# Optimization experiments

Measured on AMD Instinct MI355X. Metric: run time of the kernel, lower is better.

The kernel has to match this reference:

```python
import jax, jax.numpy as jnp
import numpy as np

N, E, SEQ, IN, HID, OUT = 2048, 65536, 5, 32, 64, 16
EPS = 1e-5


def setup_inputs() -> dict:
    ks = jax.random.split(jax.random.key(0), 16)
    def w(k, shape):
        return jax.random.normal(k, shape, jnp.float32) / np.float32(np.sqrt(shape[0]))
    z = lambda n: jnp.zeros((n,), jnp.float32)
    return dict(
        x=jax.random.normal(ks[0], (SEQ, N, IN), jnp.float32),
        edge_weight=jax.random.uniform(ks[1], (E,), jnp.float32),
        Wcz=w(ks[2], (IN, HID)), bcz=z(HID), Wlz=w(ks[3], (2 * HID, HID)), blz=z(HID),
        Wcr=w(ks[4], (IN, HID)), bcr=z(HID), Wlr=w(ks[5], (2 * HID, HID)), blr=z(HID),
        Wch=w(ks[6], (IN, HID)), bch=z(HID), Wlh=w(ks[7], (2 * HID, HID)), blh=z(HID),
        Wred=w(ks[8], (SEQ * HID, HID)), bred=z(HID),
        Wc1=w(ks[9], (HID, HID)), bc1=z(HID), Wc2=w(ks[10], (HID, HID)), bc2=z(HID),
        g1=jnp.ones((HID,), jnp.float32), be1=z(HID),
        g2=jnp.ones((HID,), jnp.float32), be2=z(HID),
        Wout=w(ks[11], (HID, OUT)), bout=z(OUT),
        Wi1=w(ks[12], (2 * HID, HID)), bi1=z(HID),
        Wi2=w(ks[13], (HID, 1)), bi2=z(1),
        edge_index=jax.random.randint(ks[14], (2, E), 0, N),
    )


def _layer_norm(h, g, b):
    mu = jnp.mean(h, -1, keepdims=True)
    var = jnp.mean((h - mu) ** 2, -1, keepdims=True)
    return (h - mu) * jax.lax.rsqrt(var + EPS) * g + b


def _forward(x, edge_weight, Wcz, bcz, Wlz, blz, Wcr, bcr, Wlr, blr,
             Wch, bch, Wlh, blh, Wred, bred, Wc1, bc1, Wc2, bc2,
             g1, be1, g2, be2, Wout, bout, Wi1, bi1, Wi2, bi2, edge_index):
    src, dst = edge_index[0], edge_index[1]
    # GCN symmetric normalization with self-loops (weight 1.0); shared by all convs.
    deg = jax.ops.segment_sum(edge_weight, dst, num_segments=N) + 1.0
    dinv = jax.lax.rsqrt(deg)
    norm = dinv[src] * edge_weight * dinv[dst]  # [E]
    dself = dinv * dinv                          # [N] self-loop coefficient

    def gcn(h, W, b):
        hw = h @ W
        agg = jax.ops.segment_sum(norm[:, None] * hw[src], dst, num_segments=N)
        return agg + dself[:, None] * hw + b

    # TGCN per timestep. The original passes no hidden state, so H resets to 0
    # each call: H_t = (1 - Z) * tanh(candidate); reset gate R is multiplied by
    # H=0 and has no effect (its params get zero gradient, matching torch).
    hs = []
    for t in range(SEQ):  # SEQ=5, fixed small loop
        Zg = jax.nn.sigmoid(gcn(x[t], Wcz, bcz) @ Wlz[:HID] + blz)
        Ht = jnp.tanh(gcn(x[t], Wch, bch) @ Wlh[:HID] + blh)
        hs.append((1.0 - Zg) * Ht)
    h = jnp.stack(hs, axis=1).reshape(N, SEQ * HID)
    h = h @ Wred + bred
    emb = h  # intermediate embeddings for the interaction predictor
    h = gcn(h, Wc1, bc1)
    h = jax.nn.relu(_layer_norm(h, g1, be1))  # dropout = identity in eval
    h = gcn(h, Wc2, bc2)
    h = jax.nn.relu(_layer_norm(h, g2, be2))
    node_pred = h @ Wout + bout
    # InteractionPredictor: cat([e_i, e_j]) @ Wi1 == e_i @ Wi1[:H] + e_j @ Wi1[H:]
    a = emb @ Wi1[:HID]
    bj = emb @ Wi1[HID:]
    hp = jax.nn.relu(a[:, None, :] + bj[None, :, :] + bi1)  # [N, N, HID]
    scores = (hp @ Wi2)[..., 0] + bi2[0]                     # [N, N]
    return node_pred, scores


def reference(x, edge_index, edge_weight, Wcz, bcz, Wlz, blz, Wcr, bcr, Wlr, blr,
              Wch, bch, Wlh, blh, Wred, bred, Wc1, bc1, Wc2, bc2,
              g1, be1, g2, be2, Wout, bout, Wi1, bi1, Wi2, bi2):
    return _forward(x, edge_weight, Wcz, bcz, Wlz, blz, Wcr, bcr, Wlr, blr,
                    Wch, bch, Wlh, blh, Wred, bred, Wc1, bc1, Wc2, bc2,
                    g1, be1, g2, be2, Wout, bout, Wi1, bi1, Wi2, bi2, edge_index)
```

## Files before the change

### kernel.cpp

```cpp
#include <hip/hip_runtime.h>
#include <math.h>

#define N_NODES 2048
#define N_EDGES 65536
#define SEQL 5
#define IN_F 32
#define HID 64
#define OUT_F 16
#define LN_EPS 1e-5f

__global__ void k_deg(const int* __restrict__ ei, const float* __restrict__ ew,
                      float* __restrict__ deg, int* __restrict__ cnt){
    int e = blockIdx.x * 256 + threadIdx.x;
    if (e < N_EDGES){
        int d = ei[N_EDGES + e];
        atomicAdd(&deg[d], ew[e]);
        atomicAdd(&cnt[d], 1);
    }
}

__global__ void k_scan_wcomb(const float* __restrict__ deg, const int* __restrict__ cnt,
                             float* __restrict__ dinv, float* __restrict__ dself, int* __restrict__ rowptr,
                             const float* __restrict__ Wcz, const float* __restrict__ Wlz,
                             const float* __restrict__ bcz, const float* __restrict__ blz,
                             const float* __restrict__ Wch, const float* __restrict__ Wlh,
                             const float* __restrict__ bch, const float* __restrict__ blh,
                             float* __restrict__ Wzp, float* __restrict__ Whp, float* __restrict__ bUV){
    int b = blockIdx.x, t = threadIdx.x;
    if (b == 0){
        __shared__ int s[1024];
        int n0 = 2*t, n1 = 2*t + 1;
        float d0 = deg[n0] + 1.f, d1 = deg[n1] + 1.f;
        float i0 = 1.f / sqrtf(d0), i1 = 1.f / sqrtf(d1);
        dinv[n0] = i0; dinv[n1] = i1;
        dself[n0] = i0*i0; dself[n1] = i1*i1;
        int a0 = cnt[n0], a1 = cnt[n1];
        s[t] = a0 + a1;
        __syncthreads();
        for (int off = 1; off < 1024; off <<= 1){
            int v = (t >= off) ? s[t - off] : 0;
            __syncthreads();
            s[t] += v;
            __syncthreads();
        }
        int pe = (t == 0) ? 0 : s[t-1];
        rowptr[n0] = pe;
        rowptr[n1] = pe + a0;
        if (t == 1023) rowptr[2048] = s[1023];
    } else {
        const float* Wc = (b == 1) ? Wcz : Wch;
        const float* Wl = (b == 1) ? Wlz : Wlh;
        const float* bc = (b == 1) ? bcz : bch;
        const float* bl = (b == 1) ? blz : blh;
        float* Wp = (b == 1) ? Wzp : Whp;
        for (int idx = t; idx < IN_F*HID; idx += 1024){
            int i = idx >> 6, f = idx & 63;
            float s = 0.f;
            for (int k = 0; k < HID; ++k) s += Wc[i*HID+k] * Wl[k*HID+f];
            Wp[idx] = s;
        }
        if (t < HID){
            float s = bl[t];
            for (int k = 0; k < HID; ++k) s += bc[k] * Wl[k*HID+t];
            bUV[(b-1)*HID + t] = s;
        }
    }
}

__global__ void k_csr(const int* __restrict__ ei, const float* __restrict__ ew,
                      const float* __restrict__ dinv, const int* __restrict__ rowptr,
                      int* __restrict__ fill, int* __restrict__ csrc, float* __restrict__ cnrm){
    int e = blockIdx.x * 256 + threadIdx.x;
    if (e < N_EDGES){
        int s = ei[e], d = ei[N_EDGES + e];
        int pos = rowptr[d] + atomicAdd(&fill[d], 1);
        csrc[pos] = s;
        cnrm[pos] = dinv[s] * ew[e] * dinv[d];
    }
}

__global__ void k_uv(const float* __restrict__ x, const float* __restrict__ Wzp,
                     const float* __restrict__ Whp, float* __restrict__ U, float* __restrict__ V){
    int r = blockIdx.x;
    int t = threadIdx.x;
    __shared__ float xs[IN_F];
    if (t < IN_F) xs[t] = x[r*IN_F + t];
    __syncthreads();
    int f = t & 63;
    const float* W = (t < 64) ? Wzp : Whp;
    float* O = (t < 64) ? U : V;
    float s = 0.f;
    #pragma unroll
    for (int i = 0; i < IN_F; ++i) s += xs[i] * W[i*HID + f];
    O[r*HID + f] = s;
}

__global__ __launch_bounds__(320) void k_gate(
                       const float* __restrict__ U, const float* __restrict__ V, const float* __restrict__ bUV,
                       const float* __restrict__ dself, const int* __restrict__ rowptr,
                       const int* __restrict__ csrc, const float* __restrict__ cnrm,
                       const float* __restrict__ Wred, const float* __restrict__ bred,
                       const float* __restrict__ Wi1, const float* __restrict__ bi1, const float* __restrict__ Wc1,
                       float* __restrict__ emb, float* __restrict__ ag, float* __restrict__ bjp,
                       float* __restrict__ hw1){
    int n = blockIdx.x;
    int f = threadIdx.x & 63;
    int t = threadIdx.x >> 6;
    __shared__ float hs[SEQL][HID];
    __shared__ float part[SEQL][HID];
    float ds = dself[n];
    int beg = rowptr[n], end = rowptr[n+1];
    const float* Ut = U + (size_t)t * N_NODES * HID;
    const float* Vt = V + (size_t)t * N_NODES * HID;
    float au = 0.f, av = 0.f;
    int p = beg;
    for (; p + 1 < end; p += 2){
        int   s0 = csrc[p],  s1 = csrc[p+1];
        float n0 = cnrm[p],  n1 = cnrm[p+1];
        float u0 = Ut[s0*HID+f], u1 = Ut[s1*HID+f];
        float v0 = Vt[s0*HID+f], v1 = Vt[s1*HID+f];
        au += n0*u0 + n1*u1;
        av += n0*v0 + n1*v1;
    }
    if (p < end){
        int s0 = csrc[p]; float n0 = cnrm[p];
        au += n0 * Ut[s0*HID+f];
        av += n0 * Vt[s0*HID+f];
    }
    float zz = au + ds * Ut[n*HID+f] + bUV[f];
    float hh = av + ds * Vt[n*HID+f] + bUV[HID+f];
    float z = 1.f / (1.f + expf(-zz));
    hs[t][f] = (1.f - z) * tanhf(hh);
    __syncthreads();
    float pp = 0.f;
    #pragma unroll
    for (int k = 0; k < HID; ++k) pp += hs[t][k] * Wred[(t*HID + k)*HID + f];
    part[t][f] = pp;
    __syncthreads();
    if (t == 0){
        float hred = bred[f] + part[0][f] + part[1][f] + part[2][f] + part[3][f] + part[4][f];
        emb[n*HID + f] = hred;
        hs[0][f] = hred;
    }
    __syncthreads();
    if (t < 3){
        const float* W = (t == 0) ? Wi1 : (t == 1) ? (Wi1 + HID*HID) : Wc1;
        float acc = (t == 1) ? bi1[f] : 0.f;
        #pragma unroll
        for (int k = 0; k < HID; ++k) acc += hs[0][k] * W[k*HID + f];
        float* O = (t == 0) ? ag : (t == 1) ? bjp : hw1;
        O[n*HID + f] = acc;
    }
}

__global__ __launch_bounds__(256) void k_gcn1(
                       const float* __restrict__ hw1, const float* __restrict__ dself,
                       const int* __restrict__ rowptr, const int* __restrict__ csrc, const float* __restrict__ cnrm,
                       const float* __restrict__ bc1, const float* __restrict__ g1, const float* __restrict__ be1,
                       const float* __restrict__ Wc2, float* __restrict__ hw2){
    int n = blockIdx.x;
    int f = threadIdx.x & 63;
    int w = threadIdx.x >> 6;
    int beg = rowptr[n], end = rowptr[n+1];
    __shared__ float red[4][HID];
    __shared__ float hsh[HID];
    float agg = 0.f;
    for (int p = beg + w; p < end; p += 4) agg += cnrm[p] * hw1[csrc[p]*HID + f];
    red[w][f] = agg;
    __syncthreads();
    if (w == 0){
        float g = red[0][f] + red[1][f] + red[2][f] + red[3][f]
                + dself[n] * hw1[n*HID + f] + bc1[f];
        float sum = g;
        for (int o = 32; o > 0; o >>= 1) sum += __shfl_xor(sum, o, 64);
        float mu = sum * (1.f/64.f);
        float d = g - mu;
        float vs = d * d;
        for (int o = 32; o > 0; o >>= 1) vs += __shfl_xor(vs, o, 64);
        float var = vs * (1.f/64.f);
        float h = d * (1.f / sqrtf(var + LN_EPS)) * g1[f] + be1[f];
        hsh[f] = fmaxf(h, 0.f);
    }
    __syncthreads();
    float s = 0.f;
    #pragma unroll
    for (int k = 0; k < 16; ++k) s += hsh[w*16 + k] * Wc2[(w*16 + k)*HID + f];
    red[w][f] = s;
    __syncthreads();
    if (w == 0) hw2[n*HID + f] = red[0][f] + red[1][f] + red[2][f] + red[3][f];
}

__global__ __launch_bounds__(256) void k_gcn2(
                       const float* __restrict__ hw2, const float* __restrict__ dself,
                       const int* __restrict__ rowptr, const int* __restrict__ csrc, const float* __restrict__ cnrm,
                       const float* __restrict__ bc2, const float* __restrict__ g2, const float* __restrict__ be2,
                       const float* __restrict__ Wout, const float* __restrict__ bout, float* __restrict__ outp){
    int n = blockIdx.x;
    int f = threadIdx.x & 63;
    int w = threadIdx.x >> 6;
    int beg = rowptr[n], end = rowptr[n+1];
    __shared__ float red[4][HID];
    __shared__ float hsh[HID];
    float agg = 0.f;
    for (int p = beg + w; p < end; p += 4) agg += cnrm[p] * hw2[csrc[p]*HID + f];
    red[w][f] = agg;
    __syncthreads();
    if (w == 0){
        float g = red[0][f] + red[1][f] + red[2][f] + red[3][f]
                + dself[n] * hw2[n*HID + f] + bc2[f];
        float sum = g;
        for (int o = 32; o > 0; o >>= 1) sum += __shfl_xor(sum, o, 64);
        float mu = sum * (1.f/64.f);
        float d = g - mu;
        float vs = d * d;
        for (int o = 32; o > 0; o >>= 1) vs += __shfl_xor(vs, o, 64);
        float var = vs * (1.f/64.f);
        float h = d * (1.f / sqrtf(var + LN_EPS)) * g2[f] + be2[f];
        hsh[f] = fmaxf(h, 0.f);
    }
    __syncthreads();
    if (w == 0 && f < OUT_F){
        float s = bout[f];
        #pragma unroll
        for (int k = 0; k < HID; ++k) s += hsh[k] * Wout[k*OUT_F + f];
        outp[n*OUT_F + f] = s;
    }
}

__global__ __launch_bounds__(256) void k_scores(const float* __restrict__ ag, const float* __restrict__ bjp,
                         const float* __restrict__ Wi2, const float* __restrict__ bi2,
                         float* __restrict__ outs){
    __shared__ float bs[64*65];
    __shared__ float wv[64];
    int tid = threadIdx.x;
    int j0 = blockIdx.x * 64;
    int i0 = blockIdx.y * 16;
    for (int idx = tid; idx < 4096; idx += 256){
        int jj = idx >> 6, f = idx & 63;
        bs[jj*65 + f] = bjp[(j0 + jj)*HID + f];
    }
    if (tid < 64) wv[tid] = Wi2[tid];
    __syncthreads();
    int tj = tid & 63;
    int w = __builtin_amdgcn_readfirstlane(tid >> 6);
    const float* ar = ag + (i0 + w*4)*HID;
    float bi2v = bi2[0];
    float acc0 = 0.f, acc1 = 0.f, acc2 = 0.f, acc3 = 0.f;
    #pragma unroll
    for (int f = 0; f < 64; ++f){
        float bv = bs[tj*65 + f];
        float wf = wv[f];
        acc0 += fmaxf(ar[       f] + bv, 0.f) * wf;
        acc1 += fmaxf(ar[ 64 +  f] + bv, 0.f) * wf;
        acc2 += fmaxf(ar[128 +  f] + bv, 0.f) * wf;
        acc3 += fmaxf(ar[192 +  f] + bv, 0.f) * wf;
    }
    long ro = (long)(i0 + w*4) * N_NODES + j0 + tj;
    outs[ro                ] = acc0 + bi2v;
    outs[ro +     N_NODES  ] = acc1 + bi2v;
    outs[ro + 2L* N_NODES  ] = acc2 + bi2v;
    outs[ro + 3L* N_NODES  ] = acc3 + bi2v;
}

extern "C" void kernel_launch(void* const* d_in, const int* in_sizes, int n_in,
                              void* d_out, int out_size, void* d_ws, size_t ws_size,
                              hipStream_t stream){
    const float* x   = (const float*)d_in[0];
    const float* ew  = (const float*)d_in[1];
    const float* Wcz = (const float*)d_in[2];  const float* bcz = (const float*)d_in[3];
    const float* Wlz = (const float*)d_in[4];  const float* blz = (const float*)d_in[5];
    const float* Wch = (const float*)d_in[10]; const float* bch = (const float*)d_in[11];
    const float* Wlh = (const float*)d_in[12]; const float* blh = (const float*)d_in[13];
    const float* Wred= (const float*)d_in[14]; const float* bred= (const float*)d_in[15];
    const float* Wc1 = (const float*)d_in[16]; const float* bc1 = (const float*)d_in[17];
    const float* Wc2 = (const float*)d_in[18]; const float* bc2 = (const float*)d_in[19];
    const float* g1  = (const float*)d_in[20]; const float* be1 = (const float*)d_in[21];
    const float* g2  = (const float*)d_in[22]; const float* be2 = (const float*)d_in[23];
    const float* Wout= (const float*)d_in[24]; const float* bout= (const float*)d_in[25];
    const float* Wi1 = (const float*)d_in[26]; const float* bi1 = (const float*)d_in[27];
    const float* Wi2 = (const float*)d_in[28]; const float* bi2 = (const float*)d_in[29];
    const int*  ei  = (const int*)d_in[30];

    char* w = (char*)d_ws;
    float* deg    = (float*)(w + 0);
    int*   cnt    = (int*)  (w + 8192);
    int*   fill   = (int*)  (w + 16384);
    int*   rowptr = (int*)  (w + 24576);
    float* dinv   = (float*)(w + 36864);
    float* dself  = (float*)(w + 45056);
    int*   csrc   = (int*)  (w + 53248);
    float* cnrm   = (float*)(w + 315392);
    float* Wzp    = (float*)(w + 577536);
    float* Whp    = (float*)(w + 585728);
    float* bUV    = (float*)(w + 593920);
    float* U      = (float*)(w + 595968);
    float* V      = (float*)(w + 595968 + 2621440);
    float* emb    = (float*)(w + 595968 + 2*2621440);
    float* ag     = emb + N_NODES*HID;
    float* bjp    = ag  + N_NODES*HID;
    float* hw1    = bjp + N_NODES*HID;
    float* hw2    = hw1 + N_NODES*HID;

    hipMemsetAsync(d_ws, 0, 24576, stream);
    k_deg<<<N_EDGES/256, 256, 0, stream>>>(ei, ew, deg, cnt);
    k_scan_wcomb<<<3, 1024, 0, stream>>>(deg, cnt, dinv, dself, rowptr,
                                         Wcz, Wlz, bcz, blz, Wch, Wlh, bch, blh,
                                         Wzp, Whp, bUV);
    k_csr<<<N_EDGES/256, 256, 0, stream>>>(ei, ew, dinv, rowptr, fill, csrc, cnrm);
    k_uv<<<SEQL*N_NODES, 128, 0, stream>>>(x, Wzp, Whp, U, V);
    k_gate<<<N_NODES, 320, 0, stream>>>(U, V, bUV, dself, rowptr, csrc, cnrm,
                                        Wred, bred, Wi1, bi1, Wc1,
                                        emb, ag, bjp, hw1);
    k_gcn1<<<N_NODES, 256, 0, stream>>>(hw1, dself, rowptr, csrc, cnrm, bc1, g1, be1, Wc2, hw2);
    k_gcn2<<<N_NODES, 256, 0, stream>>>(hw2, dself, rowptr, csrc, cnrm, bc2, g2, be2, Wout, bout,
                                        (float*)d_out);
    dim3 sg(N_NODES/64, N_NODES/16);
    k_scores<<<sg, 256, 0, stream>>>(ag, bjp, Wi2, bi2, (float*)d_out + N_NODES*OUT_F);
}
```

Baseline: 231.7 us.

## Aggregate raw inputs before projection and vectorize scores kernel LDS loads

Uses the linearity of the GCN to aggregate the 32-wide input features over neighbours first (k_aggx), then applies the combined Z/H projections inside the gate kernel. This drops the separate U/V projection kernel and halves the gather width from two 64-wide tensors per timestep to one 32-wide tensor, removing the U/V intermediate buffers. The scores kernel also stages the ag rows in shared memory with float4 loads and reads operands as float4 from padded LDS. The trade-off is extra per-node projection arithmetic in the gate kernel, plus floating-point summation order changing slightly.

```diff
diff --git a/kernel.cpp b/kernel.cpp
--- a/kernel.cpp
+++ b/kernel.cpp
@@ -79,56 +79,54 @@
     }
 }
 
-__global__ void k_uv(const float* __restrict__ x, const float* __restrict__ Wzp,
-                     const float* __restrict__ Whp, float* __restrict__ U, float* __restrict__ V){
-    int r = blockIdx.x;
-    int t = threadIdx.x;
-    __shared__ float xs[IN_F];
-    if (t < IN_F) xs[t] = x[r*IN_F + t];
-    __syncthreads();
-    int f = t & 63;
-    const float* W = (t < 64) ? Wzp : Whp;
-    float* O = (t < 64) ? U : V;
-    float s = 0.f;
-    #pragma unroll
-    for (int i = 0; i < IN_F; ++i) s += xs[i] * W[i*HID + f];
-    O[r*HID + f] = s;
-}
-
-__global__ __launch_bounds__(320) void k_gate(
-                       const float* __restrict__ U, const float* __restrict__ V, const float* __restrict__ bUV,
-                       const float* __restrict__ dself, const int* __restrict__ rowptr,
-                       const int* __restrict__ csrc, const float* __restrict__ cnrm,
-                       const float* __restrict__ Wred, const float* __restrict__ bred,
-                       const float* __restrict__ Wi1, const float* __restrict__ bi1, const float* __restrict__ Wc1,
-                       float* __restrict__ emb, float* __restrict__ ag, float* __restrict__ bjp,
-                       float* __restrict__ hw1){
+__global__ __launch_bounds__(256) void k_aggx(const float* __restrict__ x, const float* __restrict__ dself,
+        const int* __restrict__ rowptr, const int* __restrict__ csrc, const float* __restrict__ cnrm,
+        float* __restrict__ aggX){
+    int n = blockIdx.x;
+    int tid = threadIdx.x;
+    int slot = tid >> 5, f = tid & 31;
+    __shared__ float part[8][SEQL][IN_F];
+    float acc[SEQL] = {0.f, 0.f, 0.f, 0.f, 0.f};
+    int beg = rowptr[n], end = rowptr[n+1];
+    for (int p = beg + slot; p < end; p += 8){
+        int s = csrc[p]; float c = cnrm[p];
+        #pragma unroll
+        for (int t = 0; t < SEQL; ++t)
+            acc[t] += c * x[(t*N_NODES + s)*IN_F + f];
+    }
+    #pragma unroll
+    for (int t = 0; t < SEQL; ++t) part[slot][t][f] = acc[t];
+    __syncthreads();
+    if (tid < SEQL*IN_F){
+        int t = tid >> 5, ff = tid & 31;
+        float s = dself[n] * x[(t*N_NODES + n)*IN_F + ff];
+        #pragma unroll
+        for (int sl = 0; sl < 8; ++sl) s += part[sl][t][ff];
+        aggX[n*(SEQL*IN_F) + tid] = s;
+    }
+}
+
+__global__ __launch_bounds__(320) void k_gate2(const float* __restrict__ aggX, const float* __restrict__ bUV,
+        const float* __restrict__ Wzp, const float* __restrict__ Whp,
+        const float* __restrict__ Wred, const float* __restrict__ bred,
+        const float* __restrict__ Wi1, const float* __restrict__ bi1, const float* __restrict__ Wc1,
+        float* __restrict__ emb, float* __restrict__ ag, float* __restrict__ bjp,
+        float* __restrict__ hw1){
     int n = blockIdx.x;
     int f = threadIdx.x & 63;
     int t = threadIdx.x >> 6;
+    __shared__ float axs[SEQL][IN_F];
     __shared__ float hs[SEQL][HID];
     __shared__ float part[SEQL][HID];
-    float ds = dself[n];
-    int beg = rowptr[n], end = rowptr[n+1];
-    const float* Ut = U + (size_t)t * N_NODES * HID;
-    const float* Vt = V + (size_t)t * N_NODES * HID;
-    float au = 0.f, av = 0.f;
-    int p = beg;
-    for (; p + 1 < end; p += 2){
-        int   s0 = csrc[p],  s1 = csrc[p+1];
-        float n0 = cnrm[p],  n1 = cnrm[p+1];
-        float u0 = Ut[s0*HID+f], u1 = Ut[s1*HID+f];
-        float v0 = Vt[s0*HID+f], v1 = Vt[s1*HID+f];
-        au += n0*u0 + n1*u1;
-        av += n0*v0 + n1*v1;
-    }
-    if (p < end){
-        int s0 = csrc[p]; float n0 = cnrm[p];
-        au += n0 * Ut[s0*HID+f];
-        av += n0 * Vt[s0*HID+f];
-    }
-    float zz = au + ds * Ut[n*HID+f] + bUV[f];
-    float hh = av + ds * Vt[n*HID+f] + bUV[HID+f];
+    if (threadIdx.x < SEQL*IN_F) ((float*)axs)[threadIdx.x] = aggX[n*(SEQL*IN_F) + threadIdx.x];
+    __syncthreads();
+    float zz = bUV[f], hh = bUV[HID + f];
+    #pragma unroll
+    for (int i = 0; i < IN_F; ++i){
+        float a = axs[t][i];
+        zz += a * Wzp[i*HID + f];
+        hh += a * Whp[i*HID + f];
+    }
     float z = 1.f / (1.f + expf(-zz));
     hs[t][f] = (1.f - z) * tanhf(hh);
     __syncthreads();
@@ -230,30 +228,43 @@
 __global__ __launch_bounds__(256) void k_scores(const float* __restrict__ ag, const float* __restrict__ bjp,
                          const float* __restrict__ Wi2, const float* __restrict__ bi2,
                          float* __restrict__ outs){
-    __shared__ float bs[64*65];
-    __shared__ float wv[64];
+    __shared__ __align__(16) float bs[64][68];
+    __shared__ __align__(16) float as[16][68];
+    __shared__ __align__(16) float wv[64];
     int tid = threadIdx.x;
     int j0 = blockIdx.x * 64;
     int i0 = blockIdx.y * 16;
-    for (int idx = tid; idx < 4096; idx += 256){
-        int jj = idx >> 6, f = idx & 63;
-        bs[jj*65 + f] = bjp[(j0 + jj)*HID + f];
+    for (int idx = tid; idx < 1024; idx += 256){
+        int jj = idx >> 4, c = idx & 15;
+        float4 v = *(const float4*)&bjp[(j0 + jj)*HID + c*4];
+        *(float4*)&bs[jj][c*4] = v;
+    }
+    {   int ii = tid >> 4, c = tid & 15;
+        float4 v = *(const float4*)&ag[(i0 + ii)*HID + c*4];
+        *(float4*)&as[ii][c*4] = v;
     }
     if (tid < 64) wv[tid] = Wi2[tid];
     __syncthreads();
     int tj = tid & 63;
-    int w = __builtin_amdgcn_readfirstlane(tid >> 6);
-    const float* ar = ag + (i0 + w*4)*HID;
+    int w = tid >> 6;
     float bi2v = bi2[0];
     float acc0 = 0.f, acc1 = 0.f, acc2 = 0.f, acc3 = 0.f;
     #pragma unroll
-    for (int f = 0; f < 64; ++f){
-        float bv = bs[tj*65 + f];
-        float wf = wv[f];
-        acc0 += fmaxf(ar[       f] + bv, 0.f) * wf;
-        acc1 += fmaxf(ar[ 64 +  f] + bv, 0.f) * wf;
-        acc2 += fmaxf(ar[128 +  f] + bv, 0.f) * wf;
-        acc3 += fmaxf(ar[192 +  f] + bv, 0.f) * wf;
+    for (int c = 0; c < 16; ++c){
+        float4 bv = *(float4*)&bs[tj][c*4];
+        float4 w4 = *(float4*)&wv[c*4];
+        float4 a0 = *(float4*)&as[w*4 + 0][c*4];
+        float4 a1 = *(float4*)&as[w*4 + 1][c*4];
+        float4 a2 = *(float4*)&as[w*4 + 2][c*4];
+        float4 a3 = *(float4*)&as[w*4 + 3][c*4];
+        acc0 += fmaxf(a0.x+bv.x,0.f)*w4.x + fmaxf(a0.y+bv.y,0.f)*w4.y
+              + fmaxf(a0.z+bv.z,0.f)*w4.z + fmaxf(a0.w+bv.w,0.f)*w4.w;
+        acc1 += fmaxf(a1.x+bv.x,0.f)*w4.x + fmaxf(a1.y+bv.y,0.f)*w4.y
+              + fmaxf(a1.z+bv.z,0.f)*w4.z + fmaxf(a1.w+bv.w,0.f)*w4.w;
+        acc2 += fmaxf(a2.x+bv.x,0.f)*w4.x + fmaxf(a2.y+bv.y,0.f)*w4.y
+              + fmaxf(a2.z+bv.z,0.f)*w4.z + fmaxf(a2.w+bv.w,0.f)*w4.w;
+        acc3 += fmaxf(a3.x+bv.x,0.f)*w4.x + fmaxf(a3.y+bv.y,0.f)*w4.y
+              + fmaxf(a3.z+bv.z,0.f)*w4.z + fmaxf(a3.w+bv.w,0.f)*w4.w;
     }
     long ro = (long)(i0 + w*4) * N_NODES + j0 + tj;
     outs[ro                ] = acc0 + bi2v;
@@ -293,9 +304,8 @@
     float* Wzp    = (float*)(w + 577536);
     float* Whp    = (float*)(w + 585728);
     float* bUV    = (float*)(w + 593920);
-    float* U      = (float*)(w + 595968);
-    float* V      = (float*)(w + 595968 + 2621440);
-    float* emb    = (float*)(w + 595968 + 2*2621440);
+    float* aggX   = (float*)(w + 595968);
+    float* emb    = (float*)(w + 1906688);
     float* ag     = emb + N_NODES*HID;
     float* bjp    = ag  + N_NODES*HID;
     float* hw1    = bjp + N_NODES*HID;
@@ -307,10 +317,9 @@
                                          Wcz, Wlz, bcz, blz, Wch, Wlh, bch, blh,
                                          Wzp, Whp, bUV);
     k_csr<<<N_EDGES/256, 256, 0, stream>>>(ei, ew, dinv, rowptr, fill, csrc, cnrm);
-    k_uv<<<SEQL*N_NODES, 128, 0, stream>>>(x, Wzp, Whp, U, V);
-    k_gate<<<N_NODES, 320, 0, stream>>>(U, V, bUV, dself, rowptr, csrc, cnrm,
-                                        Wred, bred, Wi1, bi1, Wc1,
-                                        emb, ag, bjp, hw1);
+    k_aggx<<<N_NODES, 256, 0, stream>>>(x, dself, rowptr, csrc, cnrm, aggX);
+    k_gate2<<<N_NODES, 320, 0, stream>>>(aggX, bUV, Wzp, Whp, Wred, bred, Wi1, bi1, Wc1,
+                                         emb, ag, bjp, hw1);
     k_gcn1<<<N_NODES, 256, 0, stream>>>(hw1, dself, rowptr, csrc, cnrm, bc1, g1, be1, Wc2, hw2);
     k_gcn2<<<N_NODES, 256, 0, stream>>>(hw2, dself, rowptr, csrc, cnrm, bc2, g2, be2, Wout, bout,
                                         (float*)d_out);
```

Measured after the change: 218.8 us. 5.6% less time.

## Aggregate raw inputs before projection and fuse degree/scan setup into one block

Applied to the files above, without the earlier changes.

The gate kernel now aggregates the 32-wide raw x features over neighbors and applies the combined weights afterward (A·x·W instead of A·(x·W)). This removes the k_uv kernel and the large U/V intermediate buffers, and it halves the gathered width. The degree histogram and count now run in shared-memory atomics inside a single block of the new setup kernel, which replaces the memset, k_deg and the separate scan kernel. The fill buffer is zeroed by an extra block. The trade-off is that 64K edges are now processed serially by one 1024-thread block, and the projection matmuls move into the per-node gate kernel.

```diff
diff --git a/kernel.cpp b/kernel.cpp
--- a/kernel.cpp
+++ b/kernel.cpp
@@ -9,45 +9,50 @@
 #define OUT_F 16
 #define LN_EPS 1e-5f
 
-__global__ void k_deg(const int* __restrict__ ei, const float* __restrict__ ew,
-                      float* __restrict__ deg, int* __restrict__ cnt){
-    int e = blockIdx.x * 256 + threadIdx.x;
-    if (e < N_EDGES){
-        int d = ei[N_EDGES + e];
-        atomicAdd(&deg[d], ew[e]);
-        atomicAdd(&cnt[d], 1);
-    }
-}
-
-__global__ void k_scan_wcomb(const float* __restrict__ deg, const int* __restrict__ cnt,
-                             float* __restrict__ dinv, float* __restrict__ dself, int* __restrict__ rowptr,
-                             const float* __restrict__ Wcz, const float* __restrict__ Wlz,
-                             const float* __restrict__ bcz, const float* __restrict__ blz,
-                             const float* __restrict__ Wch, const float* __restrict__ Wlh,
-                             const float* __restrict__ bch, const float* __restrict__ blh,
-                             float* __restrict__ Wzp, float* __restrict__ Whp, float* __restrict__ bUV){
+__global__ __launch_bounds__(1024) void k_setup(
+        const int* __restrict__ ei, const float* __restrict__ ew,
+        const float* __restrict__ Wcz, const float* __restrict__ Wlz,
+        const float* __restrict__ bcz, const float* __restrict__ blz,
+        const float* __restrict__ Wch, const float* __restrict__ Wlh,
+        const float* __restrict__ bch, const float* __restrict__ blh,
+        int* __restrict__ rowptr, float* __restrict__ dinv, float* __restrict__ dself,
+        int* __restrict__ fill,
+        float* __restrict__ Wzp, float* __restrict__ Whp, float* __restrict__ bUV){
     int b = blockIdx.x, t = threadIdx.x;
     if (b == 0){
-        __shared__ int s[1024];
-        int n0 = 2*t, n1 = 2*t + 1;
-        float d0 = deg[n0] + 1.f, d1 = deg[n1] + 1.f;
-        float i0 = 1.f / sqrtf(d0), i1 = 1.f / sqrtf(d1);
-        dinv[n0] = i0; dinv[n1] = i1;
-        dself[n0] = i0*i0; dself[n1] = i1*i1;
-        int a0 = cnt[n0], a1 = cnt[n1];
-        s[t] = a0 + a1;
+        __shared__ int   hist[N_NODES];
+        __shared__ float degs[N_NODES];
+        __shared__ int   sc[1024];
+        hist[t] = 0; hist[t + 1024] = 0;
+        degs[t] = 0.f; degs[t + 1024] = 0.f;
+        __syncthreads();
+        #pragma unroll 4
+        for (int i = 0; i < 64; ++i){
+            int e = t + i*1024;
+            int d = ei[N_EDGES + e];
+            atomicAdd(&hist[d], 1);
+            atomicAdd(&degs[d], ew[e]);
+        }
+        __syncthreads();
+        int c0 = hist[2*t], c1 = hist[2*t+1];
+        int ts = c0 + c1;
+        sc[t] = ts;
         __syncthreads();
         for (int off = 1; off < 1024; off <<= 1){
-            int v = (t >= off) ? s[t - off] : 0;
+            int v = (t >= off) ? sc[t - off] : 0;
             __syncthreads();
-            s[t] += v;
+            sc[t] += v;
             __syncthreads();
         }
-        int pe = (t == 0) ? 0 : s[t-1];
-        rowptr[n0] = pe;
-        rowptr[n1] = pe + a0;
-        if (t == 1023) rowptr[2048] = s[1023];
-    } else {
+        int exc = sc[t] - ts;
+        rowptr[2*t]   = exc;
+        rowptr[2*t+1] = exc + c0;
+        if (t == 1023) rowptr[N_NODES] = sc[t];
+        float i0 = 1.f / sqrtf(degs[2*t] + 1.f);
+        float i1 = 1.f / sqrtf(degs[2*t+1] + 1.f);
+        dinv[2*t] = i0;   dinv[2*t+1] = i1;
+        dself[2*t] = i0*i0; dself[2*t+1] = i1*i1;
+    } else if (b == 1 || b == 2){
         const float* Wc = (b == 1) ? Wcz : Wch;
         const float* Wl = (b == 1) ? Wlz : Wlh;
         const float* bc = (b == 1) ? bcz : bch;
@@ -64,6 +69,8 @@
             for (int k = 0; k < HID; ++k) s += bc[k] * Wl[k*HID+t];
             bUV[(b-1)*HID + t] = s;
         }
+    } else {
+        if (t < N_NODES/2){ fill[2*t] = 0; fill[2*t+1] = 0; }
     }
 }
 
@@ -79,75 +86,76 @@
     }
 }
 
-__global__ void k_uv(const float* __restrict__ x, const float* __restrict__ Wzp,
-                     const float* __restrict__ Whp, float* __restrict__ U, float* __restrict__ V){
-    int r = blockIdx.x;
-    int t = threadIdx.x;
-    __shared__ float xs[IN_F];
-    if (t < IN_F) xs[t] = x[r*IN_F + t];
-    __syncthreads();
-    int f = t & 63;
-    const float* W = (t < 64) ? Wzp : Whp;
-    float* O = (t < 64) ? U : V;
-    float s = 0.f;
-    #pragma unroll
-    for (int i = 0; i < IN_F; ++i) s += xs[i] * W[i*HID + f];
-    O[r*HID + f] = s;
-}
-
-__global__ __launch_bounds__(320) void k_gate(
-                       const float* __restrict__ U, const float* __restrict__ V, const float* __restrict__ bUV,
-                       const float* __restrict__ dself, const int* __restrict__ rowptr,
-                       const int* __restrict__ csrc, const float* __restrict__ cnrm,
-                       const float* __restrict__ Wred, const float* __restrict__ bred,
-                       const float* __restrict__ Wi1, const float* __restrict__ bi1, const float* __restrict__ Wc1,
-                       float* __restrict__ emb, float* __restrict__ ag, float* __restrict__ bjp,
-                       float* __restrict__ hw1){
+__global__ __launch_bounds__(320) void k_gate(const float* __restrict__ x,
+        const float* __restrict__ dself, const int* __restrict__ rowptr,
+        const int* __restrict__ csrc, const float* __restrict__ cnrm,
+        const float* __restrict__ bUV, const float* __restrict__ Wzp, const float* __restrict__ Whp,
+        const float* __restrict__ Wred, const float* __restrict__ bred,
+        const float* __restrict__ Wi1, const float* __restrict__ bi1, const float* __restrict__ Wc1,
+        float* __restrict__ ag, float* __restrict__ bjp, float* __restrict__ hw1){
     int n = blockIdx.x;
-    int f = threadIdx.x & 63;
-    int t = threadIdx.x >> 6;
+    int tid = threadIdx.x;
+    __shared__ float part[10][SEQL][IN_F];
+    __shared__ float axs[SEQL][IN_F];
     __shared__ float hs[SEQL][HID];
-    __shared__ float part[SEQL][HID];
-    float ds = dself[n];
+    __shared__ float pw[SEQL][HID];
+    __shared__ float hemb[HID];
+    const int slot = tid >> 5, f5 = tid & 31;
+    const int f = tid & 63, t = tid >> 6;
     int beg = rowptr[n], end = rowptr[n+1];
-    const float* Ut = U + (size_t)t * N_NODES * HID;
-    const float* Vt = V + (size_t)t * N_NODES * HID;
-    float au = 0.f, av = 0.f;
-    int p = beg;
-    for (; p + 1 < end; p += 2){
-        int   s0 = csrc[p],  s1 = csrc[p+1];
-        float n0 = cnrm[p],  n1 = cnrm[p+1];
-        float u0 = Ut[s0*HID+f], u1 = Ut[s1*HID+f];
-        float v0 = Vt[s0*HID+f], v1 = Vt[s1*HID+f];
-        au += n0*u0 + n1*u1;
-        av += n0*v0 + n1*v1;
-    }
-    if (p < end){
-        int s0 = csrc[p]; float n0 = cnrm[p];
-        au += n0 * Ut[s0*HID+f];
-        av += n0 * Vt[s0*HID+f];
-    }
-    float zz = au + ds * Ut[n*HID+f] + bUV[f];
-    float hh = av + ds * Vt[n*HID+f] + bUV[HID+f];
-    float z = 1.f / (1.f + expf(-zz));
-    hs[t][f] = (1.f - z) * tanhf(hh);
-    __syncthreads();
-    float pp = 0.f;
-    #pragma unroll
-    for (int k = 0; k < HID; ++k) pp += hs[t][k] * Wred[(t*HID + k)*HID + f];
-    part[t][f] = pp;
-    __syncthreads();
-    if (t == 0){
-        float hred = bred[f] + part[0][f] + part[1][f] + part[2][f] + part[3][f] + part[4][f];
-        emb[n*HID + f] = hred;
-        hs[0][f] = hred;
+    float a0=0.f, a1=0.f, a2=0.f, a3=0.f, a4=0.f;
+    for (int p = beg + slot; p < end; p += 10){
+        int s = csrc[p]; float c = cnrm[p];
+        a0 += c * x[(0*N_NODES + s)*IN_F + f5];
+        a1 += c * x[(1*N_NODES + s)*IN_F + f5];
+        a2 += c * x[(2*N_NODES + s)*IN_F + f5];
+        a3 += c * x[(3*N_NODES + s)*IN_F + f5];
+        a4 += c * x[(4*N_NODES + s)*IN_F + f5];
+    }
+    part[slot][0][f5] = a0;
+    part[slot][1][f5] = a1;
+    part[slot][2][f5] = a2;
+    part[slot][3][f5] = a3;
+    part[slot][4][f5] = a4;
+    __syncthreads();
+    if (tid < SEQL*IN_F){
+        int tt = tid >> 5, ff = tid & 31;
+        float s = dself[n] * x[(tt*N_NODES + n)*IN_F + ff];
+        #pragma unroll
+        for (int sl = 0; sl < 10; ++sl) s += part[sl][tt][ff];
+        axs[tt][ff] = s;
+    }
+    __syncthreads();
+    {
+        float zz = bUV[f], hh = bUV[HID + f];
+        #pragma unroll
+        for (int i = 0; i < IN_F; ++i){
+            float a = axs[t][i];
+            zz += a * Wzp[i*HID + f];
+            hh += a * Whp[i*HID + f];
+        }
+        float z = 1.f / (1.f + expf(-zz));
+        hs[t][f] = (1.f - z) * tanhf(hh);
+    }
+    __syncthreads();
+    {   float pp = 0.f;
+        #pragma unroll
+        for (int k = 0; k < HID; ++k) pp += hs[t][k] * Wred[(t*HID + k)*HID + f];
+        pw[t][f] = pp;
+    }
+    __syncthreads();
+    if (tid < HID){
+        float hr = bred[tid];
+        #pragma unroll
+        for (int t2 = 0; t2 < SEQL; ++t2) hr += pw[t2][tid];
+        hemb[tid] = hr;
     }
     __syncthreads();
     if (t < 3){
         const float* W = (t == 0) ? Wi1 : (t == 1) ? (Wi1 + HID*HID) : Wc1;
         float acc = (t == 1) ? bi1[f] : 0.f;
         #pragma unroll
-        for (int k = 0; k < HID; ++k) acc += hs[0][k] * W[k*HID + f];
+        for (int k = 0; k < HID; ++k) acc += hemb[k] * W[k*HID + f];
         float* O = (t == 0) ? ag : (t == 1) ? bjp : hw1;
         O[n*HID + f] = acc;
     }
@@ -281,36 +289,26 @@
     const float* Wi2 = (const float*)d_in[28]; const float* bi2 = (const float*)d_in[29];
     const int*  ei  = (const int*)d_in[30];
 
-    char* w = (char*)d_ws;
-    float* deg    = (float*)(w + 0);
-    int*   cnt    = (int*)  (w + 8192);
-    int*   fill   = (int*)  (w + 16384);
-    int*   rowptr = (int*)  (w + 24576);
-    float* dinv   = (float*)(w + 36864);
-    float* dself  = (float*)(w + 45056);
-    int*   csrc   = (int*)  (w + 53248);
-    float* cnrm   = (float*)(w + 315392);
-    float* Wzp    = (float*)(w + 577536);
-    float* Whp    = (float*)(w + 585728);
-    float* bUV    = (float*)(w + 593920);
-    float* U      = (float*)(w + 595968);
-    float* V      = (float*)(w + 595968 + 2621440);
-    float* emb    = (float*)(w + 595968 + 2*2621440);
-    float* ag     = emb + N_NODES*HID;
-    float* bjp    = ag  + N_NODES*HID;
-    float* hw1    = bjp + N_NODES*HID;
-    float* hw2    = hw1 + N_NODES*HID;
-
-    hipMemsetAsync(d_ws, 0, 24576, stream);
-    k_deg<<<N_EDGES/256, 256, 0, stream>>>(ei, ew, deg, cnt);
-    k_scan_wcomb<<<3, 1024, 0, stream>>>(deg, cnt, dinv, dself, rowptr,
-                                         Wcz, Wlz, bcz, blz, Wch, Wlh, bch, blh,
-                                         Wzp, Whp, bUV);
+    float* w = (float*)d_ws;
+    int*   rowptr = (int*)w;
+    float* dinv   = w + 2560;
+    float* dself  = w + 4608;
+    int*   fill   = (int*)(w + 6656);
+    int*   csrc   = (int*)(w + 8704);
+    float* cnrm   = w + 74240;
+    float* Wzp    = w + 139776;
+    float* Whp    = w + 141824;
+    float* bUV    = w + 143872;
+    float* ag     = w + 144000;
+    float* bjp    = w + 275072;
+    float* hw1    = w + 406144;
+    float* hw2    = w + 537216;
+
+    k_setup<<<4, 1024, 0, stream>>>(ei, ew, Wcz, Wlz, bcz, blz, Wch, Wlh, bch, blh,
+                                    rowptr, dinv, dself, fill, Wzp, Whp, bUV);
     k_csr<<<N_EDGES/256, 256, 0, stream>>>(ei, ew, dinv, rowptr, fill, csrc, cnrm);
-    k_uv<<<SEQL*N_NODES, 128, 0, stream>>>(x, Wzp, Whp, U, V);
-    k_gate<<<N_NODES, 320, 0, stream>>>(U, V, bUV, dself, rowptr, csrc, cnrm,
-                                        Wred, bred, Wi1, bi1, Wc1,
-                                        emb, ag, bjp, hw1);
+    k_gate<<<N_NODES, 320, 0, stream>>>(x, dself, rowptr, csrc, cnrm, bUV, Wzp, Whp,
+                                        Wred, bred, Wi1, bi1, Wc1, ag, bjp, hw1);
     k_gcn1<<<N_NODES, 256, 0, stream>>>(hw1, dself, rowptr, csrc, cnrm, bc1, g1, be1, Wc2, hw2);
     k_gcn2<<<N_NODES, 256, 0, stream>>>(hw2, dself, rowptr, csrc, cnrm, bc2, g2, be2, Wout, bout,
                                         (float*)d_out);
```

After: 288.0 us. 1.24x slower.
